# Kernel tuning notes

Hardware: AMD Instinct MI355X
Metric: run time of the kernel (lower is better)

Reference implementation:

```python
import jax, jax.numpy as jnp
import numpy as np
import math

N, E = 50000, 800000
N_BASIS, N_ATOM, L = 32, 128, 2
START, STOP = 0.0, 10.0

_idx = [(i, j, L - i - j) for i in range(L + 1) for j in range(L + 1 - i)]
IP = np.array([t[0] for t in _idx], np.float32)
JP = np.array([t[1] for t in _idx], np.float32)
KP = np.array([t[2] for t in _idx], np.float32)
_d = np.array([math.factorial(a) * math.factorial(b) * math.factorial(c) for a, b, c in _idx], np.float32)
PREF2 = np.sqrt(math.factorial(L) / _d).astype(np.float32)  # [T], T = (L+1)(L+2)/2 = 6
OFFSETS = np.linspace(START, STOP, N_BASIS, dtype=np.float32)
WIDTH = np.float32(OFFSETS[1] - OFFSETS[0])


def _signed_pow(x, p):
    # matches torch.pow for negative base with integer-valued float exponent
    p = np.asarray(p)
    odd = (p.astype(np.int64) % 2 == 1)
    r = jnp.abs(x)[:, None] ** jnp.asarray(p)[None, :]
    return jnp.where((x < 0.0)[:, None] & jnp.asarray(odd)[None, :], -r, r)


def setup_inputs() -> dict:
    key = jax.random.key(0)
    ks = jax.random.split(key, 12)
    s = 0.05
    return {
        "feat": jax.random.normal(ks[0], (N, N_ATOM), jnp.float32),
        "dis_vec": jax.random.normal(ks[1], (E, 3), jnp.float32),
        "cj_w1": jax.random.normal(ks[2], (N_ATOM, N_ATOM), jnp.float32) * s,
        "cj_b1": jnp.zeros((N_ATOM,), jnp.float32),
        "cj_w2": jax.random.normal(ks[3], (N_ATOM, 1), jnp.float32) * s,
        "cj_b2": jnp.zeros((1,), jnp.float32),
        "msg_w1": jax.random.normal(ks[4], (N_BASIS, N_ATOM), jnp.float32) * s,
        "msg_b1": jnp.zeros((N_ATOM,), jnp.float32),
        "msg_w2": jax.random.normal(ks[5], (N_ATOM, N_ATOM), jnp.float32) * s,
        "msg_b2": jnp.zeros((N_ATOM,), jnp.float32),
        "filt_w1": jax.random.normal(ks[6], (IP.shape[0], IP.shape[0]), jnp.float32) * s,
        "filt_w2": jax.random.normal(ks[7], (IP.shape[0], 1), jnp.float32) * s,
        "filt_b2": jnp.zeros((1,), jnp.float32),
        "src": jax.random.randint(ks[8], (E,), 0, N, jnp.int32),
        "dst": jax.random.randint(ks[9], (E,), 0, N, jnp.int32),
    }


def reference(feat, dis_vec, cj_w1, cj_b1, cj_w2, cj_b2, msg_w1, msg_b1, msg_w2, msg_b2, filt_w1, filt_w2, filt_b2, src, dst):
    silu = jax.nn.silu  # swish
    # polynomial prefactor: [E, T]
    phix = _signed_pow(dis_vec[:, 0] + 1e-8, IP)
    phiy = _signed_pow(dis_vec[:, 1] + 1e-8, JP)
    phiz = _signed_pow(dis_vec[:, 2] + 1e-8, KP)
    prefactor = phix * phiy * phiz
    # gaussian basis: [E, n_basis] (cutoff_network is None -> C = 1)
    dis = jnp.linalg.norm(dis_vec + 1e-9, axis=-1)
    coeff = -0.5 / (WIDTH ** 2)
    g0 = jnp.exp(coeff * (dis[:, None] - jnp.asarray(OFFSETS)[None, :]) ** 2)
    # gauss: [E, n_basis, T]
    gauss = prefactor[:, None, :] * g0[:, :, None] * jnp.asarray(PREF2)[None, None, :]
    # cj = cj_mlp(feat): [N, 1]
    cj = silu(feat @ cj_w1 + cj_b1) @ cj_w2 + cj_b2
    # e_mul_v: gather dst-node scalar onto edges; copy_e_sum(g.reverse()): scatter-sum to src nodes
    fij = gauss * cj[dst][:, :, None]  # [E, n_basis, T]
    agg = jax.ops.segment_sum(fij, src, num_segments=N)  # [N, n_basis, T]
    f2 = jnp.sum(agg ** 2, axis=-1)  # [N, n_basis]
    msg_in = f2 / (jnp.linalg.norm(f2 + 1e-9, axis=-1, keepdims=True) + 1.0)
    msg_out = silu(msg_in @ msg_w1 + msg_b1) @ msg_w2 + msg_b2  # [N, n_atom_basis]
    gn = gauss / (jnp.linalg.norm(gauss + 1e-8, axis=-1) + 1.0)[..., None]
    filt = (silu(gn @ filt_w1) @ filt_w2 + filt_b2)[..., 0]  # [E, n_basis]
    return msg_out, filt
```

## Files before the change

### kernel.cpp

```cpp
#include <hip/hip_runtime.h>
#include <math.h>

#define N_NODES 50000
#define N_EDGES 800000
#define NB 32
#define NA 128
#define CJ_BLOCKS 782
#define CNT_BLOCKS 3125
#define EDGE_BLOCKS 3125
#define SCAN_BLOCKS 49
#define AGG_BLOCKS 782

constexpr double STEP_D = 10.0 / 31.0;
constexpr float  STEP_F = (float)(10.0 / 31.0);
constexpr float  COEFF  = -0.5f / (STEP_F * STEP_F);
constexpr float  R2     = 1.41421356237309515f;
constexpr float  INV_STEP = 3.1f;
constexpr float  HWIN   = 2.05f;

__device__ __forceinline__ float fast_rcp(float x) {
    return __builtin_amdgcn_rcpf(x);
}

__device__ __forceinline__ float silu_f(float x) {
    return x * fast_rcp(1.0f + __expf(-x));
}

__global__ __launch_bounds__(256) void k_cj_count(const float* __restrict__ feat,
                                                  const float* __restrict__ w1,
                                                  const float* __restrict__ b1,
                                                  const float* __restrict__ w2,
                                                  const float* __restrict__ b2,
                                                  float* __restrict__ cj,
                                                  const int* __restrict__ src,
                                                  int* __restrict__ cnt) {
    __shared__ float fls[64 * 128];
    int tid = threadIdx.x;
    int blk = blockIdx.x;
    if (blk >= CJ_BLOCKS) {
        int e = (blk - CJ_BLOCKS) * 256 + tid;
        if (e < N_EDGES) atomicAdd(&cnt[src[e]], 1);
        return;
    }
    int jq  = tid & 31;
    int ng  = tid >> 5;
    int j0  = jq * 4;
    int n0  = blk * 64;

    {
        const float4* fp = (const float4*)feat;
        int base = n0 * 32;
        int maxi = N_NODES * 32 - 1;
#pragma unroll
        for (int r = 0; r < 8; r++) {
            int idx = base + r * 256 + tid;
            ((float4*)fls)[r * 256 + tid] = fp[min(idx, maxi)];
        }
    }
    __syncthreads();

    float4 bv = *(const float4*)&b1[j0];
    float h[8][4];
#pragma unroll
    for (int i = 0; i < 8; i++) {
        h[i][0] = bv.x; h[i][1] = bv.y; h[i][2] = bv.z; h[i][3] = bv.w;
    }
    for (int kb = 0; kb < 128; kb += 4) {
        float4 wv[4];
#pragma unroll
        for (int u = 0; u < 4; u++) wv[u] = *(const float4*)&w1[(kb + u) * 128 + j0];
#pragma unroll
        for (int i = 0; i < 8; i++) {
            float4 f4 = *(const float4*)&fls[(ng * 8 + i) * 128 + kb];
            h[i][0] = fmaf(f4.x, wv[0].x, h[i][0]);
            h[i][1] = fmaf(f4.x, wv[0].y, h[i][1]);
            h[i][2] = fmaf(f4.x, wv[0].z, h[i][2]);
            h[i][3] = fmaf(f4.x, wv[0].w, h[i][3]);
            h[i][0] = fmaf(f4.y, wv[1].x, h[i][0]);
            h[i][1] = fmaf(f4.y, wv[1].y, h[i][1]);
            h[i][2] = fmaf(f4.y, wv[1].z, h[i][2]);
            h[i][3] = fmaf(f4.y, wv[1].w, h[i][3]);
            h[i][0] = fmaf(f4.z, wv[2].x, h[i][0]);
            h[i][1] = fmaf(f4.z, wv[2].y, h[i][1]);
            h[i][2] = fmaf(f4.z, wv[2].z, h[i][2]);
            h[i][3] = fmaf(f4.z, wv[2].w, h[i][3]);
            h[i][0] = fmaf(f4.w, wv[3].x, h[i][0]);
            h[i][1] = fmaf(f4.w, wv[3].y, h[i][1]);
            h[i][2] = fmaf(f4.w, wv[3].z, h[i][2]);
            h[i][3] = fmaf(f4.w, wv[3].w, h[i][3]);
        }
    }
    float4 w2v = *(const float4*)&w2[j0];
    float keep = 0.f;
#pragma unroll
    for (int i = 0; i < 8; i++) {
        float v = silu_f(h[i][0]) * w2v.x + silu_f(h[i][1]) * w2v.y
                + silu_f(h[i][2]) * w2v.z + silu_f(h[i][3]) * w2v.w;
#pragma unroll
        for (int m = 1; m < 32; m <<= 1) v += __shfl_xor(v, m, 64);
        if (jq == i) keep = v;
    }
    if (jq < 8) {
        int n = n0 + ng * 8 + jq;
        if (n < N_NODES) cj[n] = b2[0] + keep;
    }
}

__global__ __launch_bounds__(1024) void k_scan(const int* __restrict__ cnt,
                                               int* __restrict__ offs,
                                               int* __restrict__ cursor,
                                               int* __restrict__ bsum) {
    __shared__ int s[1024];
    __shared__ int sbase;
    int bid = blockIdx.x;
    int i = bid * 1024 + threadIdx.x;
    int v = (i < N_NODES) ? cnt[i] : 0;
    s[threadIdx.x] = v;
    __syncthreads();
    for (int o = 1; o < 1024; o <<= 1) {
        int t = (threadIdx.x >= (unsigned)o) ? s[threadIdx.x - o] : 0;
        __syncthreads();
        s[threadIdx.x] += t;
        __syncthreads();
    }
    if (threadIdx.x == 1023) atomicExch(&bsum[bid], s[1023] + 1);
    if (threadIdx.x < 64) {
        int lane = threadIdx.x;
        int val = 0;
        if (lane < bid) {
            int t;
            do { t = atomicAdd(&bsum[lane], 0); } while (t == 0);
            val = t - 1;
        }
#pragma unroll
        for (int m = 1; m < 64; m <<= 1) val += __shfl_xor(val, m, 64);
        if (lane == 0) sbase = val;
    }
    __syncthreads();
    if (i < N_NODES) {
        int o2 = s[threadIdx.x] - v + sbase;
        offs[i] = o2;
        cursor[i] = o2;
    }
}

__global__ __launch_bounds__(256) void k_edge(const int* __restrict__ src,
                                              const int* __restrict__ dst,
                                              const float* __restrict__ dis_vec,
                                              const float* __restrict__ cj,
                                              int* __restrict__ cursor,
                                              float* __restrict__ sedge,
                                              const float* __restrict__ fw1,
                                              const float* __restrict__ fw2,
                                              const float* __restrict__ fb2,
                                              float* __restrict__ outf) {
    __shared__ float buf[256 * 36];
    int tid = threadIdx.x;
    int e = blockIdx.x * 256 + tid;
    int se = src[e];
    int de = dst[e];
    float dx = dis_vec[3 * e], dy = dis_vec[3 * e + 1], dz = dis_vec[3 * e + 2];
    float cjd = cj[de];
    int p = atomicAdd(&cursor[se], 1);

    float ax = dx + 1e-9f, ay = dy + 1e-9f, az = dz + 1e-9f;
    float dis = sqrtf(ax * ax + ay * ay + az * az);
    float x = dx + 1e-8f, y = dy + 1e-8f, z = dz + 1e-8f;
    float pre[6];
    pre[0] = z * z;      pre[1] = y * z * R2; pre[2] = y * y;
    pre[3] = x * z * R2; pre[4] = x * y * R2; pre[5] = x * x;

    {
        float4* op = (float4*)(sedge + (size_t)p * 8);
        op[0] = make_float4(dis, pre[0] * cjd, pre[1] * cjd, pre[2] * cjd);
        op[1] = make_float4(pre[3] * cjd, pre[4] * cjd, pre[5] * cjd, 0.f);
    }

    float A = 0.f, B = 0.f;
#pragma unroll
    for (int t = 0; t < 6; t++) { A = fmaf(pre[t], pre[t], A); B += pre[t]; }
    float q[6];
#pragma unroll
    for (int tp = 0; tp < 6; tp++) {
        float s = 0.f;
#pragma unroll
        for (int t = 0; t < 6; t++) s = fmaf(pre[t], fw1[t * 6 + tp], s);
        q[tp] = s;
    }
    float bias = fb2[0];
    float w2r[6];
#pragma unroll
    for (int t = 0; t < 6; t++) w2r[t] = fw2[t];

    float* row = &buf[tid * 36];
    float4 b4v = make_float4(bias, bias, bias, bias);
#pragma unroll
    for (int r = 0; r < 8; r++) ((float4*)row)[r] = b4v;

    int b_lo = (int)ceilf((dis - HWIN) * INV_STEP);
#pragma unroll
    for (int k = 0; k < 14; k++) {
        int b = b_lo + k;
        float offb = (float)((double)b * STEP_D);
        float dd = dis - offb;
        float g = __expf(COEFF * dd * dd);
        float ns = fmaf(g * g, A, fmaf(2e-8f * g, B, 6e-16f));
        float rn = fast_rcp(sqrtf(ns) + 1.0f);
        float s = g * rn;
        float o = bias;
#pragma unroll
        for (int tp = 0; tp < 6; tp++) o = fmaf(silu_f(s * q[tp]), w2r[tp], o);
        if ((unsigned)b < 32u) row[b] = o;
    }
    __syncthreads();

    float4* ob = (float4*)(outf + (size_t)blockIdx.x * (256 * 32));
#pragma unroll
    for (int r = 0; r < 8; r++) {
        int g = r * 256 + tid;
        int eloc = g >> 3, j = g & 7;
        ob[g] = *(const float4*)&buf[eloc * 36 + j * 4];
    }
}

__global__ __launch_bounds__(256) void k_aggmsg(const float* __restrict__ sedge,
                                                const int* __restrict__ offs,
                                                const int* __restrict__ cnt,
                                                const float* __restrict__ w1,
                                                const float* __restrict__ b1,
                                                const float* __restrict__ w2,
                                                const float* __restrict__ b2,
                                                float* __restrict__ out) {
    __shared__ float mi[64 * 32];
    __shared__ float sh[64 * 128];
    int tid = threadIdx.x;
    int wv = tid >> 6, lane = tid & 63;
    int n0 = blockIdx.x * 64;
    int b = lane >> 1, th = lane & 1;
    float offb = (float)((double)b * STEP_D);
    const float4* sp4 = (const float4*)sedge;

    int pn = n0 + wv * 16 + (lane & 15);
    int pbeg = 0, pdeg = 0;
    if (pn < N_NODES) { pbeg = offs[pn]; pdeg = cnt[pn]; }

    for (int u = 0; u < 16; u++) {
        int beg = __shfl(pbeg, u, 64);
        int deg = __shfl(pdeg, u, 64);
        float a0 = 0.f, a1 = 0.f, a2 = 0.f;
        for (int c0 = 0; c0 < deg; c0 += 32) {
            int rem = deg - c0;
            int m = rem < 32 ? rem : 32;
            int li = lane < 2 * m ? lane : 2 * m - 1;
            float4 r = sp4[(size_t)(beg + c0) * 2 + li];
            float v0 = (lane & 1) ? r.x : r.y;
            float v1 = (lane & 1) ? r.y : r.z;
            float v2 = (lane & 1) ? r.z : r.w;
            for (int e2 = 0; e2 < m; e2++) {
                int sl = 2 * e2;
                float dis = __shfl(r.x, sl, 64);
                float w0 = __shfl(v0, sl + th, 64);
                float w1v = __shfl(v1, sl + th, 64);
                float w2v = __shfl(v2, sl + th, 64);
                float dd = dis - offb;
                float g = __expf(COEFF * dd * dd);
                a0 = fmaf(g, w0, a0);
                a1 = fmaf(g, w1v, a1);
                a2 = fmaf(g, w2v, a2);
            }
        }
        float s2 = a0 * a0 + a1 * a1 + a2 * a2;
        float f2 = s2 + __shfl_xor(s2, 1, 64);
        float p = f2 + 1e-9f;
        p = p * p;
        float tot = p;
#pragma unroll
        for (int mm = 1; mm < 64; mm <<= 1) tot += __shfl_xor(tot, mm, 64);
        float nrm = sqrtf(0.5f * tot);
        float val = f2 * fast_rcp(nrm + 1.0f);
        if (th == 0) mi[(wv * 16 + u) * 32 + b] = val;
    }
    __syncthreads();

    int jq  = tid & 31;
    int ng  = tid >> 5;
    int j0  = jq * 4;

    float4 b1v = *(const float4*)&b1[j0];
    float h[8][4];
#pragma unroll
    for (int i = 0; i < 8; i++) {
        h[i][0] = b1v.x; h[i][1] = b1v.y; h[i][2] = b1v.z; h[i][3] = b1v.w;
    }
#pragma unroll
    for (int bb = 0; bb < 32; bb += 4) {
        float4 wvv[4];
#pragma unroll
        for (int u = 0; u < 4; u++) wvv[u] = *(const float4*)&w1[(bb + u) * 128 + j0];
#pragma unroll
        for (int i = 0; i < 8; i++) {
            float4 m4 = *(const float4*)&mi[(ng * 8 + i) * 32 + bb];
            h[i][0] = fmaf(m4.x, wvv[0].x, h[i][0]);
            h[i][1] = fmaf(m4.x, wvv[0].y, h[i][1]);
            h[i][2] = fmaf(m4.x, wvv[0].z, h[i][2]);
            h[i][3] = fmaf(m4.x, wvv[0].w, h[i][3]);
            h[i][0] = fmaf(m4.y, wvv[1].x, h[i][0]);
            h[i][1] = fmaf(m4.y, wvv[1].y, h[i][1]);
            h[i][2] = fmaf(m4.y, wvv[1].z, h[i][2]);
            h[i][3] = fmaf(m4.y, wvv[1].w, h[i][3]);
            h[i][0] = fmaf(m4.z, wvv[2].x, h[i][0]);
            h[i][1] = fmaf(m4.z, wvv[2].y, h[i][1]);
            h[i][2] = fmaf(m4.z, wvv[2].z, h[i][2]);
            h[i][3] = fmaf(m4.z, wvv[2].w, h[i][3]);
            h[i][0] = fmaf(m4.w, wvv[3].x, h[i][0]);
            h[i][1] = fmaf(m4.w, wvv[3].y, h[i][1]);
            h[i][2] = fmaf(m4.w, wvv[3].z, h[i][2]);
            h[i][3] = fmaf(m4.w, wvv[3].w, h[i][3]);
        }
    }
#pragma unroll
    for (int i = 0; i < 8; i++) {
        float4 sv = make_float4(silu_f(h[i][0]), silu_f(h[i][1]),
                                silu_f(h[i][2]), silu_f(h[i][3]));
        *(float4*)&sh[(ng * 8 + i) * 128 + j0] = sv;
    }
    __syncthreads();

    float4 b2v = *(const float4*)&b2[j0];
    float acc[8][4];
#pragma unroll
    for (int i = 0; i < 8; i++) {
        acc[i][0] = b2v.x; acc[i][1] = b2v.y; acc[i][2] = b2v.z; acc[i][3] = b2v.w;
    }
    for (int hb = 0; hb < 128; hb += 4) {
        float4 wvv[4];
#pragma unroll
        for (int u = 0; u < 4; u++) wvv[u] = *(const float4*)&w2[(hb + u) * 128 + j0];
#pragma unroll
        for (int i = 0; i < 8; i++) {
            float4 s4 = *(const float4*)&sh[(ng * 8 + i) * 128 + hb];
            acc[i][0] = fmaf(s4.x, wvv[0].x, acc[i][0]);
            acc[i][1] = fmaf(s4.x, wvv[0].y, acc[i][1]);
            acc[i][2] = fmaf(s4.x, wvv[0].z, acc[i][2]);
            acc[i][3] = fmaf(s4.x, wvv[0].w, acc[i][3]);
            acc[i][0] = fmaf(s4.y, wvv[1].x, acc[i][0]);
            acc[i][1] = fmaf(s4.y, wvv[1].y, acc[i][1]);
            acc[i][2] = fmaf(s4.y, wvv[1].z, acc[i][2]);
            acc[i][3] = fmaf(s4.y, wvv[1].w, acc[i][3]);
            acc[i][0] = fmaf(s4.z, wvv[2].x, acc[i][0]);
            acc[i][1] = fmaf(s4.z, wvv[2].y, acc[i][1]);
            acc[i][2] = fmaf(s4.z, wvv[2].z, acc[i][2]);
            acc[i][3] = fmaf(s4.z, wvv[2].w, acc[i][3]);
            acc[i][0] = fmaf(s4.w, wvv[3].x, acc[i][0]);
            acc[i][1] = fmaf(s4.w, wvv[3].y, acc[i][1]);
            acc[i][2] = fmaf(s4.w, wvv[3].z, acc[i][2]);
            acc[i][3] = fmaf(s4.w, wvv[3].w, acc[i][3]);
        }
    }
#pragma unroll
    for (int i = 0; i < 8; i++) {
        int n = n0 + ng * 8 + i;
        if (n < N_NODES) {
            *(float4*)&out[(size_t)n * 128 + j0] =
                make_float4(acc[i][0], acc[i][1], acc[i][2], acc[i][3]);
        }
    }
}

extern "C" void kernel_launch(void* const* d_in, const int* in_sizes, int n_in,
                              void* d_out, int out_size, void* d_ws, size_t ws_size,
                              hipStream_t stream) {
    (void)in_sizes; (void)n_in; (void)out_size; (void)ws_size;
    const float* feat    = (const float*)d_in[0];
    const float* dis_vec = (const float*)d_in[1];
    const float* cj_w1   = (const float*)d_in[2];
    const float* cj_b1   = (const float*)d_in[3];
    const float* cj_w2   = (const float*)d_in[4];
    const float* cj_b2   = (const float*)d_in[5];
    const float* msg_w1  = (const float*)d_in[6];
    const float* msg_b1  = (const float*)d_in[7];
    const float* msg_w2  = (const float*)d_in[8];
    const float* msg_b2  = (const float*)d_in[9];
    const float* filt_w1 = (const float*)d_in[10];
    const float* filt_w2 = (const float*)d_in[11];
    const float* filt_b2 = (const float*)d_in[12];
    const int*   src     = (const int*)d_in[13];
    const int*   dst     = (const int*)d_in[14];
    float* out = (float*)d_out;

    float* ws     = (float*)d_ws;
    float* cj     = ws;
    int*   cnt    = (int*)(cj + 50048);
    int*   bsum   = cnt + 50048;
    int*   offs   = bsum + 64;
    int*   cursor = offs + 50048;
    float* sedge  = (float*)(cursor + 50048);

    hipMemsetAsync(cnt, 0, (50048 + 64) * sizeof(int), stream);

    k_cj_count<<<CJ_BLOCKS + CNT_BLOCKS, 256, 0, stream>>>(feat, cj_w1, cj_b1, cj_w2,
                                                           cj_b2, cj, src, cnt);
    k_scan<<<SCAN_BLOCKS, 1024, 0, stream>>>(cnt, offs, cursor, bsum);
    k_edge<<<EDGE_BLOCKS, 256, 0, stream>>>(src, dst, dis_vec, cj, cursor, sedge,
                                            filt_w1, filt_w2, filt_b2,
                                            out + (size_t)N_NODES * NA);
    k_aggmsg<<<AGG_BLOCKS, 256, 0, stream>>>(sedge, offs, cnt,
                                             msg_w1, msg_b1, msg_w2, msg_b2, out);
}
```

Measured before the change: 368.5 us.

## Halve edge-kernel LDS staging, defer atomic scatter, broadcast-load edges in aggregation

The edge kernel keeps its 14 filter outputs in registers and stages them through half-sized shared memory in two passes. This cuts LDS per block and should let more blocks fit on each CU. The atomic cursor update and the sorted-edge write move to the end of the kernel, so their latency overlaps the filter math. The aggregation kernel drops the per-chunk cooperative load and shuffle broadcast. Every lane now loads the same edge records directly, 8 edges at a time with unrolling, which removes the shuffles but issues redundant uniform global loads and adds register pressure.

```diff
diff --git a/kernel.cpp b/kernel.cpp
--- a/kernel.cpp
+++ b/kernel.cpp
@@ -154,15 +154,14 @@
                                               const float* __restrict__ fw2,
                                               const float* __restrict__ fb2,
                                               float* __restrict__ outf) {
-    __shared__ float buf[256 * 36];
+    __shared__ float buf[128 * 36];
     int tid = threadIdx.x;
     int e = blockIdx.x * 256 + tid;
     int se = src[e];
     int de = dst[e];
+    float cjd = cj[de];
+
     float dx = dis_vec[3 * e], dy = dis_vec[3 * e + 1], dz = dis_vec[3 * e + 2];
-    float cjd = cj[de];
-    int p = atomicAdd(&cursor[se], 1);
-
     float ax = dx + 1e-9f, ay = dy + 1e-9f, az = dz + 1e-9f;
     float dis = sqrtf(ax * ax + ay * ay + az * az);
     float x = dx + 1e-8f, y = dy + 1e-8f, z = dz + 1e-8f;
@@ -170,12 +169,6 @@
     pre[0] = z * z;      pre[1] = y * z * R2; pre[2] = y * y;
     pre[3] = x * z * R2; pre[4] = x * y * R2; pre[5] = x * x;
 
-    {
-        float4* op = (float4*)(sedge + (size_t)p * 8);
-        op[0] = make_float4(dis, pre[0] * cjd, pre[1] * cjd, pre[2] * cjd);
-        op[1] = make_float4(pre[3] * cjd, pre[4] * cjd, pre[5] * cjd, 0.f);
-    }
-
     float A = 0.f, B = 0.f;
 #pragma unroll
     for (int t = 0; t < 6; t++) { A = fmaf(pre[t], pre[t], A); B += pre[t]; }
@@ -192,35 +185,53 @@
 #pragma unroll
     for (int t = 0; t < 6; t++) w2r[t] = fw2[t];
 
-    float* row = &buf[tid * 36];
-    float4 b4v = make_float4(bias, bias, bias, bias);
-#pragma unroll
-    for (int r = 0; r < 8; r++) ((float4*)row)[r] = b4v;
-
     int b_lo = (int)ceilf((dis - HWIN) * INV_STEP);
+
+    float os[14];
 #pragma unroll
     for (int k = 0; k < 14; k++) {
-        int b = b_lo + k;
-        float offb = (float)((double)b * STEP_D);
+        float offb = (float)((double)(b_lo + k) * STEP_D);
         float dd = dis - offb;
         float g = __expf(COEFF * dd * dd);
         float ns = fmaf(g * g, A, fmaf(2e-8f * g, B, 6e-16f));
         float rn = fast_rcp(sqrtf(ns) + 1.0f);
-        float s = g * rn;
+        float sg = g * rn;
         float o = bias;
 #pragma unroll
-        for (int tp = 0; tp < 6; tp++) o = fmaf(silu_f(s * q[tp]), w2r[tp], o);
-        if ((unsigned)b < 32u) row[b] = o;
-    }
-    __syncthreads();
-
-    float4* ob = (float4*)(outf + (size_t)blockIdx.x * (256 * 32));
-#pragma unroll
-    for (int r = 0; r < 8; r++) {
-        int g = r * 256 + tid;
-        int eloc = g >> 3, j = g & 7;
-        ob[g] = *(const float4*)&buf[eloc * 36 + j * 4];
-    }
+        for (int tp = 0; tp < 6; tp++) o = fmaf(silu_f(sg * q[tp]), w2r[tp], o);
+        os[k] = o;
+    }
+
+    int half = tid >> 7;
+    int lrow = tid & 127;
+    float4* obase = (float4*)outf + (size_t)blockIdx.x * 2048;
+#pragma unroll
+    for (int pass = 0; pass < 2; pass++) {
+        if (half == pass) {
+            float* row = &buf[lrow * 36];
+            float4 b4v = make_float4(bias, bias, bias, bias);
+#pragma unroll
+            for (int r = 0; r < 8; r++) ((float4*)row)[r] = b4v;
+#pragma unroll
+            for (int k = 0; k < 14; k++) {
+                int b = b_lo + k;
+                if ((unsigned)b < 32u) row[b] = os[k];
+            }
+        }
+        __syncthreads();
+#pragma unroll
+        for (int r = 0; r < 4; r++) {
+            int g = r * 256 + tid;
+            int eloc = g >> 3, j = g & 7;
+            obase[pass * 1024 + g] = *(const float4*)&buf[eloc * 36 + j * 4];
+        }
+        if (pass == 0) __syncthreads();
+    }
+
+    int p = atomicAdd(&cursor[se], 1);
+    float4* op = (float4*)(sedge + (size_t)p * 8);
+    op[0] = make_float4(dis, pre[0] * cjd, pre[1] * cjd, pre[2] * cjd);
+    op[1] = make_float4(pre[3] * cjd, pre[4] * cjd, pre[5] * cjd, 0.f);
 }
 
 __global__ __launch_bounds__(256) void k_aggmsg(const float* __restrict__ sedge,
@@ -238,7 +249,6 @@
     int n0 = blockIdx.x * 64;
     int b = lane >> 1, th = lane & 1;
     float offb = (float)((double)b * STEP_D);
-    const float4* sp4 = (const float4*)sedge;
 
     int pn = n0 + wv * 16 + (lane & 15);
     int pbeg = 0, pdeg = 0;
@@ -247,27 +257,38 @@
     for (int u = 0; u < 16; u++) {
         int beg = __shfl(pbeg, u, 64);
         int deg = __shfl(pdeg, u, 64);
+        const float4* sp = (const float4*)sedge + (size_t)beg * 2;
         float a0 = 0.f, a1 = 0.f, a2 = 0.f;
-        for (int c0 = 0; c0 < deg; c0 += 32) {
-            int rem = deg - c0;
-            int m = rem < 32 ? rem : 32;
-            int li = lane < 2 * m ? lane : 2 * m - 1;
-            float4 r = sp4[(size_t)(beg + c0) * 2 + li];
-            float v0 = (lane & 1) ? r.x : r.y;
-            float v1 = (lane & 1) ? r.y : r.z;
-            float v2 = (lane & 1) ? r.z : r.w;
-            for (int e2 = 0; e2 < m; e2++) {
-                int sl = 2 * e2;
-                float dis = __shfl(r.x, sl, 64);
-                float w0 = __shfl(v0, sl + th, 64);
-                float w1v = __shfl(v1, sl + th, 64);
-                float w2v = __shfl(v2, sl + th, 64);
-                float dd = dis - offb;
+        int i = 0;
+        for (; i + 8 <= deg; i += 8) {
+            float4 r[16];
+#pragma unroll
+            for (int uu = 0; uu < 16; uu++) r[uu] = sp[uu];
+            sp += 16;
+#pragma unroll
+            for (int uu = 0; uu < 8; uu++) {
+                float4 r0 = r[2 * uu], r1 = r[2 * uu + 1];
+                float dd = r0.x - offb;
                 float g = __expf(COEFF * dd * dd);
+                float w0 = th ? r1.x : r0.y;
+                float w1v = th ? r1.y : r0.z;
+                float w2v = th ? r1.z : r0.w;
                 a0 = fmaf(g, w0, a0);
                 a1 = fmaf(g, w1v, a1);
                 a2 = fmaf(g, w2v, a2);
             }
+        }
+        for (; i < deg; i++) {
+            float4 r0 = sp[0], r1 = sp[1];
+            sp += 2;
+            float dd = r0.x - offb;
+            float g = __expf(COEFF * dd * dd);
+            float w0 = th ? r1.x : r0.y;
+            float w1v = th ? r1.y : r0.z;
+            float w2v = th ? r1.z : r0.w;
+            a0 = fmaf(g, w0, a0);
+            a1 = fmaf(g, w1v, a1);
+            a2 = fmaf(g, w2v, a2);
         }
         float s2 = a0 * a0 + a1 * a1 + a2 * a2;
         float f2 = s2 + __shfl_xor(s2, 1, 64);
```

Measured after the change: 374.1 us. No clear change (+1.5%).
